# Kernel optimization log

Measured on AMD Instinct MI355X. Metric: run time of the kernel, lower is better.

The kernel has to match this reference:

```python
import jax, jax.numpy as jnp
import numpy as np

H = 128
NX = 100000
NY = 100000
E = 500000
B = 16


def _mlp(x, W1, b1, W2, b2):
    # Linear -> ReLU -> Linear -> ReLU
    return jax.nn.relu(jax.nn.relu(x @ W1 + b1) @ W2 + b2)


def _param(key, shape):
    fan_in = shape[0]
    return jax.random.normal(key, shape, jnp.float32) * (1.0 / np.sqrt(fan_in))


def setup_inputs() -> dict:
    key = jax.random.key(0)
    ks = jax.random.split(key, 12)
    edge_dst_y = jax.random.randint(ks[0], (E,), 0, NY)   # edge_index[0] -> y nodes
    edge_src_x = jax.random.randint(ks[1], (E,), 0, NX)   # edge_index[1] -> x nodes
    return {
        "h_x": jax.random.normal(ks[2], (NX, H), jnp.float32),
        "h_x_degree": jax.random.normal(ks[3], (NX, H), jnp.float32),
        "W1m": _param(ks[4], (2 * H, 2 * H)), "b1m": jnp.zeros((2 * H,), jnp.float32),
        "W2m": _param(ks[5], (2 * H, H)),     "b2m": jnp.zeros((H,), jnp.float32),
        "W1u": _param(ks[6], (2 * H, 2 * H)), "b1u": jnp.zeros((2 * H,), jnp.float32),
        "W2u": _param(ks[7], (2 * H, H)),     "b2u": jnp.zeros((H,), jnp.float32),
        "edge_index": jnp.stack([edge_dst_y, edge_src_x], axis=0),
        "x_mask": jnp.ones((NX, 1), bool),
        "y_mask": jax.random.bernoulli(ks[8], 0.9, (NY, 1)),
        "edge_mask": jnp.ones((E,), bool),
        "batch_index_x": jax.random.randint(ks[9], (NX,), 0, B),
        "batch_index_y": jax.random.randint(ks[10], (NY,), 0, B),
        "batch_size": B,
        "eps": 1,
    }


def reference(h_x, h_x_degree, W1m, b1m, W2m, b2m, W1u, b1u, W2u, b2u,
              edge_index, x_mask, y_mask, edge_mask, batch_index_x,
              batch_index_y, batch_size, eps):
    n_x = x_mask.shape[0]
    n_y = y_mask.shape[0]
    dst_y = edge_index[0]
    src_x = edge_index[1]

    # MLP over x-node features: [n_x, h]
    x_degree = _mlp(jnp.concatenate((h_x, h_x_degree), axis=-1), W1m, b1m, W2m, b2m)

    # gather per-edge messages [E, h], scatter-min to y nodes.
    # masked edges are routed to an extra sentinel segment instead of boolean
    # compression (keeps static shapes / jit compatibility).
    msg_x_to_y = x_degree[src_x]
    dst_eff = jnp.where(edge_mask, dst_y, n_y)
    next_y = jax.ops.segment_min(msg_x_to_y, dst_eff, num_segments=n_y + 1)[:n_y]
    # pyg scatter(reduce='min') leaves untouched rows at 0
    next_y = jnp.where(jnp.isinf(next_y), 0.0, next_y)

    if eps:
        # scatter-min over masked y nodes into per-graph eps [batch_size, h]
        ym = y_mask[:, 0]
        idx_y = jnp.where(ym, batch_index_y, batch_size)
        next_eps = jax.ops.segment_min(next_y, idx_y, num_segments=batch_size + 1)[:batch_size]
        next_eps = jnp.where(jnp.isinf(next_eps), 0.0, next_eps)
        next_eps_y = next_eps[batch_index_y]       # [n_y, h]
        eps_feat = next_eps_y[dst_y]               # [E, h]
        eps_feat = jnp.where(edge_mask[:, None], eps_feat, 0.0)
        msg_y_to_x = jax.ops.segment_sum(eps_feat, src_x, num_segments=n_x)
    else:
        m = next_y[dst_y]
        m = jnp.where(edge_mask[:, None], m, 0.0)
        msg_y_to_x = jax.ops.segment_sum(m, src_x, num_segments=n_x)
        next_eps = None

    next_x = _mlp(jnp.concatenate((h_x, msg_y_to_x), axis=-1), W1u, b1u, W2u, b2u)
    return (next_x, next_y, next_eps)
```

## Files before the change

kernel.cpp:

```cpp
#include <hip/hip_runtime.h>


#define NX 100000
#define NY 100000
#define NE 500000
#define NB 16
#define HD 128
#define CAP 32

typedef __attribute__((ext_vector_type(4))) float f32x4;
typedef __attribute__((ext_vector_type(8))) short short8;
typedef __attribute__((ext_vector_type(8))) __bf16 bf16x8;

__device__ __forceinline__ unsigned short f2bf(float f) {
  unsigned int u = __float_as_uint(f);
  u += 0x7FFFu + ((u >> 16) & 1u);
  return (unsigned short)(u >> 16);
}

__device__ __forceinline__ f32x4 MFMA16(short8 a, short8 b, f32x4 c) {
  return __builtin_amdgcn_mfma_f32_16x16x32_bf16(
      __builtin_bit_cast(bf16x8, a), __builtin_bit_cast(bf16x8, b), c, 0, 0, 0);
}

__device__ __forceinline__ short8 pack8(f32x4 a, f32x4 b) {
  short8 s;
#pragma unroll
  for (int j = 0; j < 4; ++j) { s[j] = (short)f2bf(a[j]); s[4 + j] = (short)f2bf(b[j]); }
  return s;
}

__device__ __forceinline__ unsigned int pkmin(unsigned int a, unsigned int b) {
  unsigned int d;
  asm("v_pk_min_u16 %0, %1, %2" : "=v"(d) : "v"(a), "v"(b));
  return d;
}

__global__ __launch_bounds__(256) void prep_kernel(
    const float* __restrict__ W1m, const float* __restrict__ W2m,
    const float* __restrict__ W1u, const float* __restrict__ W2u,
    unsigned short* __restrict__ W1mf, unsigned short* __restrict__ W2mf,
    unsigned short* __restrict__ W1uf, unsigned short* __restrict__ W2uf) {
  int t = blockIdx.x * 256 + threadIdx.x;
  const float* src;
  unsigned short* dst;
  int n, k;
  if (t < 65536) {
    k = t >> 8; n = t & 255; src = W1m + k * 256 + n; dst = W1mf;
  } else if (t < 98304) {
    t -= 65536; k = t >> 7; n = t & 127; src = W2m + k * 128 + n; dst = W2mf;
  } else if (t < 163840) {
    t -= 98304; k = t >> 8; n = t & 255; src = W1u + k * 256 + n; dst = W1uf;
  } else {
    t -= 163840; k = t >> 7; n = t & 127; src = W2u + k * 128 + n; dst = W2uf;
  }
  int nt = n >> 4, rl = n & 15, kt = k >> 5, rh = (k >> 3) & 3, j = k & 7;
  dst[(size_t)(nt * 8 + kt) * 512 + (rh * 16 + rl) * 8 + j] = f2bf(*src);
}

template <int SECOND_BF16, int OUT_BF16>
__global__ __launch_bounds__(256, 4) void mlp_kernel(
    const float* __restrict__ first, const void* __restrict__ second_v,
    const unsigned short* __restrict__ W1f, const float* __restrict__ b1,
    const unsigned short* __restrict__ W2f, const float* __restrict__ b2,
    void* __restrict__ out) {
  __shared__ char smem[32768];
  const int t = threadIdx.x;
  const int rowbase = blockIdx.x * 64;
  const int lane = t & 63;
  const int wv = t >> 6;
  const int rl = lane & 15;
  const int rh = lane >> 4;

  const unsigned short* W1w = W1f + (size_t)(wv * 4) * 8 * 512 + lane * 8;
  const unsigned short* W2w = W2f + (size_t)(wv * 2) * 8 * 512 + lane * 8;

  short8 bc[4], bn[4];
#pragma unroll
  for (int nt = 0; nt < 4; ++nt) bc[nt] = *(const short8*)(W1w + (nt * 8 + 0) * 512);

  {
    const int row = t >> 2;
    const int q = t & 3;
    int g = rowbase + row;
    g = g < NX ? g : NX - 1;
    const int swz = (row & 7) << 4;
    if (q < 2) {
      const f32x4* p = reinterpret_cast<const f32x4*>(first + (size_t)g * HD + q * 64);
#pragma unroll
      for (int j = 0; j < 4; ++j) {
        f32x4 v0 = p[4 * j], v1 = p[4 * j + 1], v2 = p[4 * j + 2], v3 = p[4 * j + 3];
        int base = row * 512 + q * 128 + j * 32;
        *(short8*)(smem + ((base) ^ swz)) = pack8(v0, v1);
        *(short8*)(smem + ((base + 16) ^ swz)) = pack8(v2, v3);
      }
    } else if (SECOND_BF16) {
      const short8* p = reinterpret_cast<const short8*>(
          (const unsigned short*)second_v + (size_t)g * HD + (q - 2) * 64);
#pragma unroll
      for (int j = 0; j < 4; ++j) {
        int base = row * 512 + q * 128 + j * 32;
        *(short8*)(smem + ((base) ^ swz)) = p[2 * j];
        *(short8*)(smem + ((base + 16) ^ swz)) = p[2 * j + 1];
      }
    } else {
      const f32x4* p = reinterpret_cast<const f32x4*>(
          (const float*)second_v + (size_t)g * HD + (q - 2) * 64);
#pragma unroll
      for (int j = 0; j < 4; ++j) {
        f32x4 v0 = p[4 * j], v1 = p[4 * j + 1], v2 = p[4 * j + 2], v3 = p[4 * j + 3];
        int base = row * 512 + q * 128 + j * 32;
        *(short8*)(smem + ((base) ^ swz)) = pack8(v0, v1);
        *(short8*)(smem + ((base + 16) ^ swz)) = pack8(v2, v3);
      }
    }
  }
  __syncthreads();

  const int aswz = (rl & 7) << 4;

  f32x4 acc[4][4];
#pragma unroll
  for (int m = 0; m < 4; ++m)
#pragma unroll
    for (int n = 0; n < 4; ++n)
#pragma unroll
      for (int r = 0; r < 4; ++r) acc[m][n][r] = 0.0f;

#pragma unroll 2
  for (int kt = 0; kt < 8; ++kt) {
    if (kt < 7) {
#pragma unroll
      for (int nt = 0; nt < 4; ++nt)
        bn[nt] = *(const short8*)(W1w + (nt * 8 + kt + 1) * 512);
    }
    short8 a[4];
#pragma unroll
    for (int m = 0; m < 4; ++m)
      a[m] = *(const short8*)(smem + (((m * 16 + rl) * 512 + kt * 64 + rh * 16) ^ aswz));
#pragma unroll
    for (int nt = 0; nt < 4; ++nt)
#pragma unroll
      for (int m = 0; m < 4; ++m) acc[m][nt] = MFMA16(a[m], bc[nt], acc[m][nt]);
#pragma unroll
    for (int nt = 0; nt < 4; ++nt) bc[nt] = bn[nt];
  }

  short8 bc2[2], bn2[2];
#pragma unroll
  for (int nt = 0; nt < 2; ++nt) bc2[nt] = *(const short8*)(W2w + (nt * 8 + 0) * 512);

  __syncthreads();

#pragma unroll
  for (int m = 0; m < 4; ++m) {
#pragma unroll
    for (int nt = 0; nt < 4; ++nt) {
      float bias = b1[wv * 64 + nt * 16 + rl];
      int col2 = (wv * 64 + nt * 16 + rl) * 2;
#pragma unroll
      for (int r = 0; r < 4; ++r) {
        float h = fmaxf(acc[m][nt][r] + bias, 0.0f);
        int rowl = m * 16 + rh * 4 + r;
        *(unsigned short*)(smem + ((rowl * 512 + col2) ^ ((rowl & 7) << 4))) = f2bf(h);
      }
    }
  }
  __syncthreads();

  f32x4 acc2[4][2];
#pragma unroll
  for (int m = 0; m < 4; ++m)
#pragma unroll
    for (int n = 0; n < 2; ++n)
#pragma unroll
      for (int r = 0; r < 4; ++r) acc2[m][n][r] = 0.0f;

#pragma unroll 2
  for (int kt = 0; kt < 8; ++kt) {
    if (kt < 7) {
#pragma unroll
      for (int nt = 0; nt < 2; ++nt)
        bn2[nt] = *(const short8*)(W2w + (nt * 8 + kt + 1) * 512);
    }
    short8 a[4];
#pragma unroll
    for (int m = 0; m < 4; ++m)
      a[m] = *(const short8*)(smem + (((m * 16 + rl) * 512 + kt * 64 + rh * 16) ^ aswz));
#pragma unroll
    for (int nt = 0; nt < 2; ++nt)
#pragma unroll
      for (int m = 0; m < 4; ++m) acc2[m][nt] = MFMA16(a[m], bc2[nt], acc2[m][nt]);
#pragma unroll
    for (int nt = 0; nt < 2; ++nt) bc2[nt] = bn2[nt];
  }

#pragma unroll
  for (int m = 0; m < 4; ++m) {
#pragma unroll
    for (int nt = 0; nt < 2; ++nt) {
      float bias = b2[wv * 32 + nt * 16 + rl];
      int col = wv * 32 + nt * 16 + rl;
#pragma unroll
      for (int r = 0; r < 4; ++r) {
        float v = fmaxf(acc2[m][nt][r] + bias, 0.0f);
        int row = rowbase + m * 16 + rh * 4 + r;
        if (row < NX) {
          if (OUT_BF16)
            ((unsigned short*)out)[(size_t)row * HD + col] = f2bf(v);
          else
            ((float*)out)[(size_t)row * HD + col] = v;
        }
      }
    }
  }
}

__global__ __launch_bounds__(256) void edge_bucket_kernel(
    const int* __restrict__ ei, const int* __restrict__ biy,
    int* __restrict__ cnt_y, int* __restrict__ cnt_xb, int* __restrict__ bucket) {
  for (int e = blockIdx.x * 256 + threadIdx.x; e < NE; e += gridDim.x * 256) {
    int dst = ei[e];
    int src = ei[NE + e];
    int b = biy[dst];
    atomicAdd(&cnt_xb[src * 16 + b], 1);
    int pos = atomicAdd(&cnt_y[dst], 1);
    if (pos < CAP) bucket[dst * CAP + pos] = src;
  }
}

__global__ __launch_bounds__(256) void next_y_kernel(
    const unsigned short* __restrict__ xdeg, const int* __restrict__ cnt_y,
    const int* __restrict__ bucket, const void* __restrict__ xmask,
    const void* __restrict__ ymask, const int* __restrict__ biy,
    float* __restrict__ outy, unsigned int* __restrict__ eps_bits) {
  __shared__ unsigned int epsl[2048];
  const int tid = threadIdx.x;
  for (int j = tid; j < 2048; j += 256) epsl[j] = 0x7F800000u;
  __syncthreads();
  const bool bytemask = (((const int*)xmask)[0] != 1);
  const int lane = tid & 63;
  const int wv = tid >> 6;
  const int q = lane >> 4;
  const int j16 = lane & 15;
  const unsigned short* xb = xdeg + j16 * 8;
  for (int y0 = blockIdx.x * 16 + wv * 4; y0 < NY; y0 += gridDim.x * 16) {
    int4 dv = *reinterpret_cast<const int4*>(cnt_y + y0);
    int d0 = dv.x < CAP ? dv.x : CAP, d1 = dv.y < CAP ? dv.y : CAP;
    int d2 = dv.z < CAP ? dv.z : CAP, d3 = dv.w < CAP ? dv.w : CAP;
    int degq = q == 0 ? d0 : q == 1 ? d1 : q == 2 ? d2 : d3;
    int dmax = d0 > d1 ? d0 : d1;
    dmax = dmax > d2 ? dmax : d2;
    dmax = dmax > d3 ? dmax : d3;
    int4 bv = *reinterpret_cast<const int4*>(biy + y0);
    int bq = q == 0 ? bv.x : q == 1 ? bv.y : q == 2 ? bv.z : bv.w;
    unsigned int ymq;
    if (bytemask) {
      unsigned int m4 = *reinterpret_cast<const unsigned int*>((const unsigned char*)ymask + y0);
      ymq = (m4 >> (q * 8)) & 0xFFu;
    } else {
      int4 m4 = *reinterpret_cast<const int4*>((const int*)ymask + y0);
      ymq = (unsigned int)(q == 0 ? m4.x : q == 1 ? m4.y : q == 2 ? m4.z : m4.w);
    }
    unsigned int amin[4];
#pragma unroll
    for (int d = 0; d < 4; ++d) amin[d] = 0x7F807F80u;
    const int* brow = bucket + (size_t)(y0 + q) * CAP;
    for (int i0 = 0; i0 < dmax; i0 += 4) {
      int4 s4 = *reinterpret_cast<const int4*>(brow + i0);
      uint4 vv[4];
      bool pr[4];
#pragma unroll
      for (int u = 0; u < 4; ++u) pr[u] = (i0 + u) < degq;
      if (pr[0]) vv[0] = *reinterpret_cast<const uint4*>(xb + (size_t)s4.x * HD);
      if (pr[1]) vv[1] = *reinterpret_cast<const uint4*>(xb + (size_t)s4.y * HD);
      if (pr[2]) vv[2] = *reinterpret_cast<const uint4*>(xb + (size_t)s4.z * HD);
      if (pr[3]) vv[3] = *reinterpret_cast<const uint4*>(xb + (size_t)s4.w * HD);
#pragma unroll
      for (int u = 0; u < 4; ++u) {
        if (pr[u]) {
          amin[0] = pkmin(amin[0], vv[u].x);
          amin[1] = pkmin(amin[1], vv[u].y);
          amin[2] = pkmin(amin[2], vv[u].z);
          amin[3] = pkmin(amin[3], vv[u].w);
        }
      }
    }
    if (degq == 0) {
#pragma unroll
      for (int d = 0; d < 4; ++d) amin[d] = 0;
    }
    f32x4 o0, o1;
#pragma unroll
    for (int d = 0; d < 2; ++d) {
      o0[2 * d]     = __uint_as_float(amin[d] << 16);
      o0[2 * d + 1] = __uint_as_float(amin[d] & 0xFFFF0000u);
      o1[2 * d]     = __uint_as_float(amin[d + 2] << 16);
      o1[2 * d + 1] = __uint_as_float(amin[d + 2] & 0xFFFF0000u);
    }
    float* orow = outy + (size_t)(y0 + q) * HD + j16 * 8;
    *reinterpret_cast<f32x4*>(orow) = o0;
    *reinterpret_cast<f32x4*>(orow + 4) = o1;
    if (ymq) {
      unsigned int* eb = &epsl[bq * HD + j16 * 8];
#pragma unroll
      for (int d = 0; d < 4; ++d) {
        atomicMin(&eb[2 * d], amin[d] << 16);
        atomicMin(&eb[2 * d + 1], amin[d] & 0xFFFF0000u);
      }
    }
  }
  __syncthreads();
  for (int j = tid; j < 2048; j += 256) atomicMin(&eps_bits[j], epsl[j]);
}

__global__ __launch_bounds__(256) void msg_kernel(
    const int* __restrict__ cnt_xb, const unsigned int* __restrict__ eps_bits,
    unsigned short* __restrict__ msg, float* __restrict__ out_eps) {
  __shared__ float epsl[2048];
  for (int j = threadIdx.x; j < 2048; j += 256) {
    unsigned int b = eps_bits[j];
    float v = (b >= 0x7F800000u) ? 0.0f : __uint_as_float(b);
    epsl[j] = v;
    if (blockIdx.x == 0) out_eps[j] = v;
  }
  __syncthreads();
  const int total4 = NX * (HD / 4);
  for (int i = blockIdx.x * 256 + threadIdx.x; i < total4; i += gridDim.x * 256) {
    int row = i >> 5;
    int h4 = (i & 31) * 4;
    const int* c = cnt_xb + row * 16;
    float s0 = 0.f, s1 = 0.f, s2 = 0.f, s3 = 0.f;
#pragma unroll
    for (int b = 0; b < 16; ++b) {
      float cb = (float)c[b];
      f32x4 e = *reinterpret_cast<const f32x4*>(&epsl[b * HD + h4]);
      s0 += cb * e[0]; s1 += cb * e[1]; s2 += cb * e[2]; s3 += cb * e[3];
    }
    unsigned long long pk = (unsigned long long)f2bf(s0) |
                            ((unsigned long long)f2bf(s1) << 16) |
                            ((unsigned long long)f2bf(s2) << 32) |
                            ((unsigned long long)f2bf(s3) << 48);
    *reinterpret_cast<unsigned long long*>(msg + (size_t)i * 4) = pk;
  }
}

extern "C" void kernel_launch(void* const* d_in, const int* in_sizes, int n_in,
                              void* d_out, int out_size, void* d_ws, size_t ws_size,
                              hipStream_t stream) {
  const float* h_x   = (const float*)d_in[0];
  const float* h_xd  = (const float*)d_in[1];
  const float* W1m   = (const float*)d_in[2];
  const float* b1m   = (const float*)d_in[3];
  const float* W2m   = (const float*)d_in[4];
  const float* b2m   = (const float*)d_in[5];
  const float* W1u   = (const float*)d_in[6];
  const float* b1u   = (const float*)d_in[7];
  const float* W2u   = (const float*)d_in[8];
  const float* b2u   = (const float*)d_in[9];
  const int*   eidx  = (const int*)d_in[10];
  const void*  xmask = d_in[11];
  const void*  ymask = d_in[12];
  const int*   biy   = (const int*)d_in[15];

  float* out = (float*)d_out;
  float* next_y   = out + (size_t)NX * HD;
  float* next_eps = out + (size_t)NX * HD + (size_t)NY * HD;

  char* ws = (char*)d_ws;
  unsigned short* xdeg_msg = (unsigned short*)(ws + 0);
  int*            cnt_y   = (int*)(ws + 25600000);
  int*            cnt_xb  = (int*)(ws + 26000000);
  int*            bucket  = (int*)(ws + 32400000);
  unsigned int*   epsbits = (unsigned int*)(ws + 45200000);
  unsigned short* W1mf    = (unsigned short*)(ws + 45208192);
  unsigned short* W2mf    = (unsigned short*)(ws + 45339264);
  unsigned short* W1uf    = (unsigned short*)(ws + 45404800);
  unsigned short* W2uf    = (unsigned short*)(ws + 45535872);

  const int mlp_grid = (NX + 63) / 64;

  hipMemsetAsync(ws + 25600000, 0, 6800000, stream);
  hipMemsetAsync(ws + 45200000, 0xFF, 8192, stream);

  prep_kernel<<<768, 256, 0, stream>>>(W1m, W2m, W1u, W2u, W1mf, W2mf, W1uf, W2uf);
  mlp_kernel<0, 1><<<mlp_grid, 256, 0, stream>>>(h_x, (const void*)h_xd,
                                                 W1mf, b1m, W2mf, b2m, (void*)xdeg_msg);
  edge_bucket_kernel<<<1954, 256, 0, stream>>>(eidx, biy, cnt_y, cnt_xb, bucket);
  next_y_kernel<<<2048, 256, 0, stream>>>(xdeg_msg, cnt_y, bucket, xmask, ymask, biy,
                                          next_y, epsbits);
  msg_kernel<<<2048, 256, 0, stream>>>(cnt_xb, epsbits, xdeg_msg, next_eps);
  mlp_kernel<1, 0><<<mlp_grid, 256, 0, stream>>>(h_x, (const void*)xdeg_msg,
                                                 W1uf, b1u, W2uf, b2u, (void*)out);
}
```

Measured before the change: 415.0 us.

## Make MLP kernel persistent over three tiles with double-buffered LDS prefetch

Each MLP block now processes three consecutive 64-row tiles instead of one. While it computes the current tile, it loads the next tile's inputs into registers in two halves and writes them into a second LDS buffer. The grid shrinks to 521 blocks, LDS use per block doubles to 64 KB, and launch bounds drop to 2 blocks per CU. The goal is to hide global-load latency behind MFMA work, at the cost of lower occupancy and a fixed grid size that depends on NX.

```diff
diff --git a/kernel.cpp b/kernel.cpp
--- a/kernel.cpp
+++ b/kernel.cpp
@@ -59,160 +59,180 @@
 }
 
 template <int SECOND_BF16, int OUT_BF16>
-__global__ __launch_bounds__(256, 4) void mlp_kernel(
+__global__ __launch_bounds__(256, 2) void mlp_kernel(
     const float* __restrict__ first, const void* __restrict__ second_v,
     const unsigned short* __restrict__ W1f, const float* __restrict__ b1,
     const unsigned short* __restrict__ W2f, const float* __restrict__ b2,
     void* __restrict__ out) {
-  __shared__ char smem[32768];
+  __shared__ char smem[65536];
   const int t = threadIdx.x;
-  const int rowbase = blockIdx.x * 64;
   const int lane = t & 63;
   const int wv = t >> 6;
   const int rl = lane & 15;
   const int rh = lane >> 4;
+  const int srow = t >> 2;
+  const int sq = t & 3;
+  const int sswz = (srow & 7) << 4;
+  const int aswz = (rl & 7) << 4;
 
   const unsigned short* W1w = W1f + (size_t)(wv * 4) * 8 * 512 + lane * 8;
   const unsigned short* W2w = W2f + (size_t)(wv * 2) * 8 * 512 + lane * 8;
 
-  short8 bc[4], bn[4];
-#pragma unroll
-  for (int nt = 0; nt < 4; ++nt) bc[nt] = *(const short8*)(W1w + (nt * 8 + 0) * 512);
-
-  {
-    const int row = t >> 2;
-    const int q = t & 3;
-    int g = rowbase + row;
+  f32x4 pf[8];
+  short8 ps[4];
+
+  auto load_half = [&](int tile, int h) {
+    int g = tile * 64 + srow;
     g = g < NX ? g : NX - 1;
-    const int swz = (row & 7) << 4;
-    if (q < 2) {
-      const f32x4* p = reinterpret_cast<const f32x4*>(first + (size_t)g * HD + q * 64);
-#pragma unroll
-      for (int j = 0; j < 4; ++j) {
-        f32x4 v0 = p[4 * j], v1 = p[4 * j + 1], v2 = p[4 * j + 2], v3 = p[4 * j + 3];
-        int base = row * 512 + q * 128 + j * 32;
-        *(short8*)(smem + ((base) ^ swz)) = pack8(v0, v1);
-        *(short8*)(smem + ((base + 16) ^ swz)) = pack8(v2, v3);
-      }
+    if (sq < 2) {
+      const f32x4* p = reinterpret_cast<const f32x4*>(first + (size_t)g * HD + sq * 64) + h * 8;
+#pragma unroll
+      for (int i = 0; i < 8; ++i) pf[i] = p[i];
     } else if (SECOND_BF16) {
       const short8* p = reinterpret_cast<const short8*>(
-          (const unsigned short*)second_v + (size_t)g * HD + (q - 2) * 64);
-#pragma unroll
-      for (int j = 0; j < 4; ++j) {
-        int base = row * 512 + q * 128 + j * 32;
-        *(short8*)(smem + ((base) ^ swz)) = p[2 * j];
-        *(short8*)(smem + ((base + 16) ^ swz)) = p[2 * j + 1];
-      }
+          (const unsigned short*)second_v + (size_t)g * HD + (sq - 2) * 64) + h * 4;
+#pragma unroll
+      for (int i = 0; i < 4; ++i) ps[i] = p[i];
     } else {
       const f32x4* p = reinterpret_cast<const f32x4*>(
-          (const float*)second_v + (size_t)g * HD + (q - 2) * 64);
-#pragma unroll
-      for (int j = 0; j < 4; ++j) {
-        f32x4 v0 = p[4 * j], v1 = p[4 * j + 1], v2 = p[4 * j + 2], v3 = p[4 * j + 3];
-        int base = row * 512 + q * 128 + j * 32;
-        *(short8*)(smem + ((base) ^ swz)) = pack8(v0, v1);
-        *(short8*)(smem + ((base + 16) ^ swz)) = pack8(v2, v3);
-      }
-    }
-  }
+          (const float*)second_v + (size_t)g * HD + (sq - 2) * 64) + h * 8;
+#pragma unroll
+      for (int i = 0; i < 8; ++i) pf[i] = p[i];
+    }
+  };
+  auto write_half = [&](char* sb, int h) {
+#pragma unroll
+    for (int c = 0; c < 4; ++c) {
+      short8 s;
+      if (SECOND_BF16 && sq >= 2) s = ps[c];
+      else s = pack8(pf[2 * c], pf[2 * c + 1]);
+      *(short8*)(sb + ((srow * 512 + sq * 128 + (h * 4 + c) * 16) ^ sswz)) = s;
+    }
+  };
+
+  const int tile0 = blockIdx.x * 3;
+  load_half(tile0, 0);
+  write_half(smem, 0);
+  load_half(tile0, 1);
+  write_half(smem, 1);
   __syncthreads();
 
-  const int aswz = (rl & 7) << 4;
-
-  f32x4 acc[4][4];
-#pragma unroll
-  for (int m = 0; m < 4; ++m)
-#pragma unroll
-    for (int n = 0; n < 4; ++n)
-#pragma unroll
-      for (int r = 0; r < 4; ++r) acc[m][n][r] = 0.0f;
+  int cur = 0;
+  for (int it = 0; it < 3; ++it) {
+    const int tile = tile0 + it;
+    const int rowbase = tile * 64;
+    char* sbc = smem + cur * 32768;
+    char* sbn = smem + (cur ^ 1) * 32768;
+    const bool more = (it < 2);
+
+    if (more) load_half(tile + 1, 0);
+
+    short8 bc[4], bn[4];
+#pragma unroll
+    for (int nt = 0; nt < 4; ++nt) bc[nt] = *(const short8*)(W1w + (nt * 8 + 0) * 512);
+
+    f32x4 acc[4][4];
+#pragma unroll
+    for (int m = 0; m < 4; ++m)
+#pragma unroll
+      for (int n = 0; n < 4; ++n)
+#pragma unroll
+        for (int r = 0; r < 4; ++r) acc[m][n][r] = 0.0f;
 
 #pragma unroll 2
-  for (int kt = 0; kt < 8; ++kt) {
-    if (kt < 7) {
+    for (int kt = 0; kt < 8; ++kt) {
+      if (kt < 7) {
+#pragma unroll
+        for (int nt = 0; nt < 4; ++nt)
+          bn[nt] = *(const short8*)(W1w + (nt * 8 + kt + 1) * 512);
+      }
+      short8 a[4];
+#pragma unroll
+      for (int m = 0; m < 4; ++m)
+        a[m] = *(const short8*)(sbc + (((m * 16 + rl) * 512 + kt * 64 + rh * 16) ^ aswz));
 #pragma unroll
       for (int nt = 0; nt < 4; ++nt)
-        bn[nt] = *(const short8*)(W1w + (nt * 8 + kt + 1) * 512);
-    }
-    short8 a[4];
+#pragma unroll
+        for (int m = 0; m < 4; ++m) acc[m][nt] = MFMA16(a[m], bc[nt], acc[m][nt]);
+#pragma unroll
+      for (int nt = 0; nt < 4; ++nt) bc[nt] = bn[nt];
+    }
+
+    short8 bc2[2], bn2[2];
+#pragma unroll
+    for (int nt = 0; nt < 2; ++nt) bc2[nt] = *(const short8*)(W2w + (nt * 8 + 0) * 512);
+
+    __syncthreads();
+
+#pragma unroll
+    for (int m = 0; m < 4; ++m) {
+#pragma unroll
+      for (int nt = 0; nt < 4; ++nt) {
+        float bias = b1[wv * 64 + nt * 16 + rl];
+        int col2 = (wv * 64 + nt * 16 + rl) * 2;
+#pragma unroll
+        for (int r = 0; r < 4; ++r) {
+          float h = fmaxf(acc[m][nt][r] + bias, 0.0f);
+          int rowl = m * 16 + rh * 4 + r;
+          *(unsigned short*)(sbc + ((rowl * 512 + col2) ^ ((rowl & 7) << 4))) = f2bf(h);
+        }
+      }
+    }
+    if (more) {
+      write_half(sbn, 0);
+      load_half(tile + 1, 1);
+    }
+    __syncthreads();
+
+    f32x4 acc2[4][2];
 #pragma unroll
     for (int m = 0; m < 4; ++m)
-      a[m] = *(const short8*)(smem + (((m * 16 + rl) * 512 + kt * 64 + rh * 16) ^ aswz));
-#pragma unroll
-    for (int nt = 0; nt < 4; ++nt)
-#pragma unroll
-      for (int m = 0; m < 4; ++m) acc[m][nt] = MFMA16(a[m], bc[nt], acc[m][nt]);
-#pragma unroll
-    for (int nt = 0; nt < 4; ++nt) bc[nt] = bn[nt];
-  }
-
-  short8 bc2[2], bn2[2];
-#pragma unroll
-  for (int nt = 0; nt < 2; ++nt) bc2[nt] = *(const short8*)(W2w + (nt * 8 + 0) * 512);
-
-  __syncthreads();
-
-#pragma unroll
-  for (int m = 0; m < 4; ++m) {
-#pragma unroll
-    for (int nt = 0; nt < 4; ++nt) {
-      float bias = b1[wv * 64 + nt * 16 + rl];
-      int col2 = (wv * 64 + nt * 16 + rl) * 2;
-#pragma unroll
-      for (int r = 0; r < 4; ++r) {
-        float h = fmaxf(acc[m][nt][r] + bias, 0.0f);
-        int rowl = m * 16 + rh * 4 + r;
-        *(unsigned short*)(smem + ((rowl * 512 + col2) ^ ((rowl & 7) << 4))) = f2bf(h);
-      }
-    }
-  }
-  __syncthreads();
-
-  f32x4 acc2[4][2];
-#pragma unroll
-  for (int m = 0; m < 4; ++m)
-#pragma unroll
-    for (int n = 0; n < 2; ++n)
-#pragma unroll
-      for (int r = 0; r < 4; ++r) acc2[m][n][r] = 0.0f;
+#pragma unroll
+      for (int n = 0; n < 2; ++n)
+#pragma unroll
+        for (int r = 0; r < 4; ++r) acc2[m][n][r] = 0.0f;
 
 #pragma unroll 2
-  for (int kt = 0; kt < 8; ++kt) {
-    if (kt < 7) {
+    for (int kt = 0; kt < 8; ++kt) {
+      if (kt < 7) {
+#pragma unroll
+        for (int nt = 0; nt < 2; ++nt)
+          bn2[nt] = *(const short8*)(W2w + (nt * 8 + kt + 1) * 512);
+      }
+      short8 a[4];
+#pragma unroll
+      for (int m = 0; m < 4; ++m)
+        a[m] = *(const short8*)(sbc + (((m * 16 + rl) * 512 + kt * 64 + rh * 16) ^ aswz));
 #pragma unroll
       for (int nt = 0; nt < 2; ++nt)
-        bn2[nt] = *(const short8*)(W2w + (nt * 8 + kt + 1) * 512);
-    }
-    short8 a[4];
-#pragma unroll
-    for (int m = 0; m < 4; ++m)
-      a[m] = *(const short8*)(smem + (((m * 16 + rl) * 512 + kt * 64 + rh * 16) ^ aswz));
-#pragma unroll
-    for (int nt = 0; nt < 2; ++nt)
-#pragma unroll
-      for (int m = 0; m < 4; ++m) acc2[m][nt] = MFMA16(a[m], bc2[nt], acc2[m][nt]);
-#pragma unroll
-    for (int nt = 0; nt < 2; ++nt) bc2[nt] = bn2[nt];
-  }
-
-#pragma unroll
-  for (int m = 0; m < 4; ++m) {
-#pragma unroll
-    for (int nt = 0; nt < 2; ++nt) {
-      float bias = b2[wv * 32 + nt * 16 + rl];
-      int col = wv * 32 + nt * 16 + rl;
-#pragma unroll
-      for (int r = 0; r < 4; ++r) {
-        float v = fmaxf(acc2[m][nt][r] + bias, 0.0f);
-        int row = rowbase + m * 16 + rh * 4 + r;
-        if (row < NX) {
-          if (OUT_BF16)
-            ((unsigned short*)out)[(size_t)row * HD + col] = f2bf(v);
-          else
-            ((float*)out)[(size_t)row * HD + col] = v;
+#pragma unroll
+        for (int m = 0; m < 4; ++m) acc2[m][nt] = MFMA16(a[m], bc2[nt], acc2[m][nt]);
+#pragma unroll
+      for (int nt = 0; nt < 2; ++nt) bc2[nt] = bn2[nt];
+    }
+
+#pragma unroll
+    for (int m = 0; m < 4; ++m) {
+#pragma unroll
+      for (int nt = 0; nt < 2; ++nt) {
+        float bias = b2[wv * 32 + nt * 16 + rl];
+        int col = wv * 32 + nt * 16 + rl;
+#pragma unroll
+        for (int r = 0; r < 4; ++r) {
+          float v = fmaxf(acc2[m][nt][r] + bias, 0.0f);
+          int row = rowbase + m * 16 + rh * 4 + r;
+          if (row < NX) {
+            if (OUT_BF16)
+              ((unsigned short*)out)[(size_t)row * HD + col] = f2bf(v);
+            else
+              ((float*)out)[(size_t)row * HD + col] = v;
+          }
         }
       }
     }
+    if (more) write_half(sbn, 1);
+    __syncthreads();
+    cur ^= 1;
   }
 }
 
@@ -378,7 +398,7 @@
   unsigned short* W1uf    = (unsigned short*)(ws + 45404800);
   unsigned short* W2uf    = (unsigned short*)(ws + 45535872);
 
-  const int mlp_grid = (NX + 63) / 64;
+  const int mlp_grid = 521;
 
   hipMemsetAsync(ws + 25600000, 0, 6800000, stream);
   hipMemsetAsync(ws + 45200000, 0xFF, 8192, stream);
```

After: 475.9 us. 14.7% more time.

## Fuse edge bucketing into first MLP and message build into second MLP

Applied to the files above, without the earlier changes.

Folds the workspace memsets into the weight prep kernel, runs edge bucketing as extra blocks of the first MLP launch, and computes the per-x message (count-weighted sum of per-graph eps) inside the second MLP's load stage instead of a separate kernel. This removes two kernel launches, two memsets and the bf16 message round-trip through global memory. In exchange the second MLP needs more shared memory and extra per-row arithmetic, and the bucketing blocks share the first launch's hardware with the MLP blocks. The global loads are also regrouped into per-thread contiguous 32-float chunks.

```diff
diff --git a/kernel.cpp b/kernel.cpp
--- a/kernel.cpp
+++ b/kernel.cpp
@@ -7,6 +7,8 @@
 #define NB 16
 #define HD 128
 #define CAP 32
+#define MLPB 1563
+#define BUCKETB 512
 
 typedef __attribute__((ext_vector_type(4))) float f32x4;
 typedef __attribute__((ext_vector_type(8))) short short8;
@@ -40,31 +42,59 @@
     const float* __restrict__ W1m, const float* __restrict__ W2m,
     const float* __restrict__ W1u, const float* __restrict__ W2u,
     unsigned short* __restrict__ W1mf, unsigned short* __restrict__ W2mf,
-    unsigned short* __restrict__ W1uf, unsigned short* __restrict__ W2uf) {
-  int t = blockIdx.x * 256 + threadIdx.x;
-  const float* src;
-  unsigned short* dst;
-  int n, k;
-  if (t < 65536) {
-    k = t >> 8; n = t & 255; src = W1m + k * 256 + n; dst = W1mf;
-  } else if (t < 98304) {
-    t -= 65536; k = t >> 7; n = t & 127; src = W2m + k * 128 + n; dst = W2mf;
-  } else if (t < 163840) {
-    t -= 98304; k = t >> 8; n = t & 255; src = W1u + k * 256 + n; dst = W1uf;
-  } else {
-    t -= 163840; k = t >> 7; n = t & 127; src = W2u + k * 128 + n; dst = W2uf;
-  }
-  int nt = n >> 4, rl = n & 15, kt = k >> 5, rh = (k >> 3) & 3, j = k & 7;
-  dst[(size_t)(nt * 8 + kt) * 512 + (rh * 16 + rl) * 8 + j] = f2bf(*src);
-}
-
-template <int SECOND_BF16, int OUT_BF16>
+    unsigned short* __restrict__ W1uf, unsigned short* __restrict__ W2uf,
+    unsigned int* __restrict__ eps_bits, int* __restrict__ cnt_base) {
+  const int TOTAL = 196608 + 2048 + NY + NX * 16;
+  for (int i = blockIdx.x * 256 + threadIdx.x; i < TOTAL; i += gridDim.x * 256) {
+    int t = i;
+    if (t < 196608) {
+      const float* src;
+      unsigned short* dst;
+      int n, k;
+      if (t < 65536) {
+        k = t >> 8; n = t & 255; src = W1m + k * 256 + n; dst = W1mf;
+      } else if (t < 98304) {
+        t -= 65536; k = t >> 7; n = t & 127; src = W2m + k * 128 + n; dst = W2mf;
+      } else if (t < 163840) {
+        t -= 98304; k = t >> 8; n = t & 255; src = W1u + k * 256 + n; dst = W1uf;
+      } else {
+        t -= 163840; k = t >> 7; n = t & 127; src = W2u + k * 128 + n; dst = W2uf;
+      }
+      int nt = n >> 4, rl = n & 15, kt = k >> 5, rh = (k >> 3) & 3, j = k & 7;
+      dst[(size_t)(nt * 8 + kt) * 512 + (rh * 16 + rl) * 8 + j] = f2bf(*src);
+      continue;
+    }
+    t -= 196608;
+    if (t < 2048) { eps_bits[t] = 0x7F800000u; continue; }
+    t -= 2048;
+    cnt_base[t] = 0;
+  }
+}
+
+template <int MODE>
 __global__ __launch_bounds__(256, 4) void mlp_kernel(
-    const float* __restrict__ first, const void* __restrict__ second_v,
+    const float* __restrict__ first, const float* __restrict__ second,
     const unsigned short* __restrict__ W1f, const float* __restrict__ b1,
     const unsigned short* __restrict__ W2f, const float* __restrict__ b2,
-    void* __restrict__ out) {
-  __shared__ char smem[32768];
+    void* __restrict__ out,
+    const unsigned int* __restrict__ eps_bits, float* __restrict__ out_eps,
+    const int* __restrict__ ei, const int* __restrict__ biy,
+    int* __restrict__ cnt_y, int* __restrict__ cnt_xb, int* __restrict__ bucket) {
+  __shared__ char smem[MODE ? 40960 : 32768];
+
+  if (MODE == 0 && blockIdx.x >= MLPB) {
+    const int bid = blockIdx.x - MLPB;
+    for (int e = bid * 256 + threadIdx.x; e < NE; e += BUCKETB * 256) {
+      int dst = ei[e];
+      int src = ei[NE + e];
+      int b = biy[dst];
+      atomicAdd(&cnt_xb[src * 16 + b], 1);
+      int pos = atomicAdd(&cnt_y[dst], 1);
+      if (pos < CAP) bucket[dst * CAP + pos] = src;
+    }
+    return;
+  }
+
   const int t = threadIdx.x;
   const int rowbase = blockIdx.x * 64;
   const int lane = t & 63;
@@ -79,40 +109,62 @@
 #pragma unroll
   for (int nt = 0; nt < 4; ++nt) bc[nt] = *(const short8*)(W1w + (nt * 8 + 0) * 512);
 
+  float* epsl = (float*)(smem + 32768);
+  if (MODE == 1) {
+    for (int j = t; j < 2048; j += 256) {
+      unsigned int b = eps_bits[j];
+      float v = (b >= 0x7F800000u) ? 0.0f : __uint_as_float(b);
+      epsl[j] = v;
+      if (blockIdx.x == 0) out_eps[j] = v;
+    }
+    __syncthreads();
+  }
+
   {
     const int row = t >> 2;
-    const int q = t & 3;
+    const int sub = t & 3;
     int g = rowbase + row;
     g = g < NX ? g : NX - 1;
     const int swz = (row & 7) << 4;
-    if (q < 2) {
-      const f32x4* p = reinterpret_cast<const f32x4*>(first + (size_t)g * HD + q * 64);
-#pragma unroll
-      for (int j = 0; j < 4; ++j) {
-        f32x4 v0 = p[4 * j], v1 = p[4 * j + 1], v2 = p[4 * j + 2], v3 = p[4 * j + 3];
-        int base = row * 512 + q * 128 + j * 32;
-        *(short8*)(smem + ((base) ^ swz)) = pack8(v0, v1);
-        *(short8*)(smem + ((base + 16) ^ swz)) = pack8(v2, v3);
-      }
-    } else if (SECOND_BF16) {
-      const short8* p = reinterpret_cast<const short8*>(
-          (const unsigned short*)second_v + (size_t)g * HD + (q - 2) * 64);
-#pragma unroll
-      for (int j = 0; j < 4; ++j) {
-        int base = row * 512 + q * 128 + j * 32;
-        *(short8*)(smem + ((base) ^ swz)) = p[2 * j];
-        *(short8*)(smem + ((base + 16) ^ swz)) = p[2 * j + 1];
-      }
+    {
+      const f32x4* p = reinterpret_cast<const f32x4*>(first + (size_t)g * HD + sub * 32);
+      f32x4 pf[8];
+#pragma unroll
+      for (int i = 0; i < 8; ++i) pf[i] = p[i];
+#pragma unroll
+      for (int c = 0; c < 4; ++c)
+        *(short8*)(smem + ((row * 512 + sub * 64 + c * 16) ^ swz)) = pack8(pf[2 * c], pf[2 * c + 1]);
+    }
+    if (MODE == 0) {
+      const f32x4* p = reinterpret_cast<const f32x4*>(second + (size_t)g * HD + sub * 32);
+      f32x4 pf[8];
+#pragma unroll
+      for (int i = 0; i < 8; ++i) pf[i] = p[i];
+#pragma unroll
+      for (int c = 0; c < 4; ++c)
+        *(short8*)(smem + ((row * 512 + 256 + sub * 64 + c * 16) ^ swz)) = pack8(pf[2 * c], pf[2 * c + 1]);
     } else {
-      const f32x4* p = reinterpret_cast<const f32x4*>(
-          (const float*)second_v + (size_t)g * HD + (q - 2) * 64);
-#pragma unroll
-      for (int j = 0; j < 4; ++j) {
-        f32x4 v0 = p[4 * j], v1 = p[4 * j + 1], v2 = p[4 * j + 2], v3 = p[4 * j + 3];
-        int base = row * 512 + q * 128 + j * 32;
-        *(short8*)(smem + ((base) ^ swz)) = pack8(v0, v1);
-        *(short8*)(smem + ((base + 16) ^ swz)) = pack8(v2, v3);
-      }
+      const int* cr = cnt_xb + (size_t)g * 16;
+      int4 c0 = *(const int4*)cr, c1 = *(const int4*)(cr + 4);
+      int4 c2 = *(const int4*)(cr + 8), c3 = *(const int4*)(cr + 12);
+      float cb[16] = {(float)c0.x, (float)c0.y, (float)c0.z, (float)c0.w,
+                      (float)c1.x, (float)c1.y, (float)c1.z, (float)c1.w,
+                      (float)c2.x, (float)c2.y, (float)c2.z, (float)c2.w,
+                      (float)c3.x, (float)c3.y, (float)c3.z, (float)c3.w};
+      f32x4 macc[8];
+#pragma unroll
+      for (int c4 = 0; c4 < 8; ++c4)
+#pragma unroll
+        for (int r = 0; r < 4; ++r) macc[c4][r] = 0.0f;
+#pragma unroll
+      for (int b = 0; b < 16; ++b) {
+        const f32x4* er = reinterpret_cast<const f32x4*>(epsl + b * HD + sub * 32);
+#pragma unroll
+        for (int c4 = 0; c4 < 8; ++c4) macc[c4] += cb[b] * er[c4];
+      }
+#pragma unroll
+      for (int c = 0; c < 4; ++c)
+        *(short8*)(smem + ((row * 512 + 256 + sub * 64 + c * 16) ^ swz)) = pack8(macc[2 * c], macc[2 * c + 1]);
     }
   }
   __syncthreads();
@@ -206,26 +258,13 @@
         float v = fmaxf(acc2[m][nt][r] + bias, 0.0f);
         int row = rowbase + m * 16 + rh * 4 + r;
         if (row < NX) {
-          if (OUT_BF16)
+          if (MODE == 0)
             ((unsigned short*)out)[(size_t)row * HD + col] = f2bf(v);
           else
             ((float*)out)[(size_t)row * HD + col] = v;
         }
       }
     }
-  }
-}
-
-__global__ __launch_bounds__(256) void edge_bucket_kernel(
-    const int* __restrict__ ei, const int* __restrict__ biy,
-    int* __restrict__ cnt_y, int* __restrict__ cnt_xb, int* __restrict__ bucket) {
-  for (int e = blockIdx.x * 256 + threadIdx.x; e < NE; e += gridDim.x * 256) {
-    int dst = ei[e];
-    int src = ei[NE + e];
-    int b = biy[dst];
-    atomicAdd(&cnt_xb[src * 16 + b], 1);
-    int pos = atomicAdd(&cnt_y[dst], 1);
-    if (pos < CAP) bucket[dst * CAP + pos] = src;
   }
 }
 
@@ -314,37 +353,6 @@
   for (int j = tid; j < 2048; j += 256) atomicMin(&eps_bits[j], epsl[j]);
 }
 
-__global__ __launch_bounds__(256) void msg_kernel(
-    const int* __restrict__ cnt_xb, const unsigned int* __restrict__ eps_bits,
-    unsigned short* __restrict__ msg, float* __restrict__ out_eps) {
-  __shared__ float epsl[2048];
-  for (int j = threadIdx.x; j < 2048; j += 256) {
-    unsigned int b = eps_bits[j];
-    float v = (b >= 0x7F800000u) ? 0.0f : __uint_as_float(b);
-    epsl[j] = v;
-    if (blockIdx.x == 0) out_eps[j] = v;
-  }
-  __syncthreads();
-  const int total4 = NX * (HD / 4);
-  for (int i = blockIdx.x * 256 + threadIdx.x; i < total4; i += gridDim.x * 256) {
-    int row = i >> 5;
-    int h4 = (i & 31) * 4;
-    const int* c = cnt_xb + row * 16;
-    float s0 = 0.f, s1 = 0.f, s2 = 0.f, s3 = 0.f;
-#pragma unroll
-    for (int b = 0; b < 16; ++b) {
-      float cb = (float)c[b];
-      f32x4 e = *reinterpret_cast<const f32x4*>(&epsl[b * HD + h4]);
-      s0 += cb * e[0]; s1 += cb * e[1]; s2 += cb * e[2]; s3 += cb * e[3];
-    }
-    unsigned long long pk = (unsigned long long)f2bf(s0) |
-                            ((unsigned long long)f2bf(s1) << 16) |
-                            ((unsigned long long)f2bf(s2) << 32) |
-                            ((unsigned long long)f2bf(s3) << 48);
-    *reinterpret_cast<unsigned long long*>(msg + (size_t)i * 4) = pk;
-  }
-}
-
 extern "C" void kernel_launch(void* const* d_in, const int* in_sizes, int n_in,
                               void* d_out, int out_size, void* d_ws, size_t ws_size,
                               hipStream_t stream) {
@@ -368,7 +376,7 @@
   float* next_eps = out + (size_t)NX * HD + (size_t)NY * HD;
 
   char* ws = (char*)d_ws;
-  unsigned short* xdeg_msg = (unsigned short*)(ws + 0);
+  unsigned short* xdeg    = (unsigned short*)(ws + 0);
   int*            cnt_y   = (int*)(ws + 25600000);
   int*            cnt_xb  = (int*)(ws + 26000000);
   int*            bucket  = (int*)(ws + 32400000);
@@ -378,18 +386,14 @@
   unsigned short* W1uf    = (unsigned short*)(ws + 45404800);
   unsigned short* W2uf    = (unsigned short*)(ws + 45535872);
 
-  const int mlp_grid = (NX + 63) / 64;
-
-  hipMemsetAsync(ws + 25600000, 0, 6800000, stream);
-  hipMemsetAsync(ws + 45200000, 0xFF, 8192, stream);
-
-  prep_kernel<<<768, 256, 0, stream>>>(W1m, W2m, W1u, W2u, W1mf, W2mf, W1uf, W2uf);
-  mlp_kernel<0, 1><<<mlp_grid, 256, 0, stream>>>(h_x, (const void*)h_xd,
-                                                 W1mf, b1m, W2mf, b2m, (void*)xdeg_msg);
-  edge_bucket_kernel<<<1954, 256, 0, stream>>>(eidx, biy, cnt_y, cnt_xb, bucket);
-  next_y_kernel<<<2048, 256, 0, stream>>>(xdeg_msg, cnt_y, bucket, xmask, ymask, biy,
+  prep_kernel<<<2048, 256, 0, stream>>>(W1m, W2m, W1u, W2u, W1mf, W2mf, W1uf, W2uf,
+                                        epsbits, cnt_y );
+  mlp_kernel<0><<<MLPB + BUCKETB, 256, 0, stream>>>(
+      h_x, h_xd, W1mf, b1m, W2mf, b2m, (void*)xdeg,
+      nullptr, nullptr, eidx, biy, cnt_y, cnt_xb, bucket);
+  next_y_kernel<<<2048, 256, 0, stream>>>(xdeg, cnt_y, bucket, xmask, ymask, biy,
                                           next_y, epsbits);
-  msg_kernel<<<2048, 256, 0, stream>>>(cnt_xb, epsbits, xdeg_msg, next_eps);
-  mlp_kernel<1, 0><<<mlp_grid, 256, 0, stream>>>(h_x, (const void*)xdeg_msg,
-                                                 W1uf, b1u, W2uf, b2u, (void*)out);
-}
+  mlp_kernel<1><<<MLPB, 256, 0, stream>>>(
+      h_x, nullptr, W1uf, b1u, W2uf, b2u, (void*)out,
+      epsbits, next_eps, nullptr, nullptr, nullptr, cnt_xb, nullptr);
+}
```

Measured after the change: 382.2 us. -7.9%, faster.
